# Kernel tuning notes

Hardware: AMD Instinct MI355X
Metric: run time of the kernel (lower is better)

The kernel has to match this reference:

```python
import jax, jax.numpy as jnp
import numpy as np

EPS = 1e-6

def rms_norm(x):
    return x * jax.lax.rsqrt(jnp.mean(x * x, axis=-1, keepdims=True) + EPS)

def setup_inputs() -> dict:
    key = jax.random.key(0)
    k_x, k_w = jax.random.split(key)
    T, B, D = 2048, 16, 1024
    x = jax.random.normal(k_x, (T, B, D), dtype=jnp.float32)
    h0 = jnp.zeros((B, D), dtype=jnp.float32)
    # xavier_uniform for W: limit = sqrt(6/(fan_in+fan_out)) = sqrt(6/(2D))
    limit = float(np.sqrt(6.0 / (2 * D)))
    W = jax.random.uniform(k_w, (D, D), dtype=jnp.float32, minval=-limit, maxval=limit)
    b = jnp.zeros((D,), dtype=jnp.float32)
    log_alpha = jnp.asarray(np.log(0.1), dtype=jnp.float32)
    return {"x": x, "h0": h0, "W": W, "b": b, "log_alpha": log_alpha}

def reference(x, h0, W, b, log_alpha):
    # x: [T,B,D], h0: [B,D], W: [D,D], b: [D], log_alpha: []
    alpha = jnp.exp(log_alpha)
    # Precompute all input projections in one big GEMM: [T,B,D]
    Wx_all = jnp.einsum('tbd,ed->tbe', x, W) + b

    def step(h, wx):
        h_new = rms_norm(h + alpha * wx)
        out = h_new * jax.nn.silu(h_new)
        return h_new, (h_new, out)

    _, (hs, outs) = jax.lax.scan(step, h0, Wx_all)
    h = jnp.concatenate([h0[None], hs], axis=0)  # [T+1,B,D]
    return outs, h
```

## Files before the change

kernel.cpp:

```cpp
#include <hip/hip_runtime.h>
#include <hip/hip_bf16.h>

#define T_STEPS 2048
#define BATCH 16
#define DIM 1024
#define EPSV 1e-6f
#define INVD (1.0f / 1024.0f)
#define SLOTF (BATCH * DIM)
#define SLOT4C (BATCH * DIM / 4)

typedef short short8 __attribute__((ext_vector_type(8)));
typedef float f32x4 __attribute__((ext_vector_type(4)));

struct alignas(16) bf16x8pack { __hip_bfloat16 v[8]; };

__device__ __forceinline__ float dot4(const float4& a, const float4& c) {
  return fmaf(a.x, c.x, fmaf(a.y, c.y, fmaf(a.z, c.z, a.w * c.w)));
}

__device__ __forceinline__ float fast_rsq(float x) {
  float r;
  asm("v_rsq_f32 %0, %1" : "=v"(r) : "v"(x));
  return r;
}

__global__ __launch_bounds__(256) void cvt_kernel(const float* __restrict__ src,
                                                  bf16x8pack* __restrict__ dst, int n8) {
  int i = blockIdx.x * blockDim.x + threadIdx.x;
  if (i >= n8) return;
  const float4* s4 = (const float4*)src + (size_t)i * 2;
  float4 a = s4[0];
  float4 b = s4[1];
  bf16x8pack p;
  p.v[0] = __float2bfloat16(a.x); p.v[1] = __float2bfloat16(a.y);
  p.v[2] = __float2bfloat16(a.z); p.v[3] = __float2bfloat16(a.w);
  p.v[4] = __float2bfloat16(b.x); p.v[5] = __float2bfloat16(b.y);
  p.v[6] = __float2bfloat16(b.z); p.v[7] = __float2bfloat16(b.w);
  dst[i] = p;
}

__global__ __launch_bounds__(256) void gemm_kernel(
    const __hip_bfloat16* __restrict__ Xb,
    const __hip_bfloat16* __restrict__ Wb,
    const float* __restrict__ bias,
    const float* __restrict__ log_alpha_p,
    float* __restrict__ hreg) {
  __shared__ __hip_bfloat16 As[128 * 32];
  __shared__ __hip_bfloat16 Bs[128 * 32];
  const int tid = threadIdx.x;
  const int wave = tid >> 6, lane = tid & 63;
  const int m0 = blockIdx.y * 128;
  const int e0 = blockIdx.x * 128;
  const int wm = (wave >> 1) * 64;
  const int wn = (wave & 1) * 64;
  const int l15 = lane & 15, l4 = lane >> 4;

  f32x4 acc[4][4] = {};

  const int srow = wave * 16 + (lane >> 2);
  const int sch = (lane & 3) * 8;

  for (int kt = 0; kt < DIM; kt += 32) {
    __syncthreads();
#pragma unroll
    for (int i = 0; i < 2; ++i) {
      const __hip_bfloat16* ga = Xb + (size_t)(m0 + i * 64 + srow) * DIM + kt + sch;
      const __hip_bfloat16* gb = Wb + (size_t)(e0 + i * 64 + srow) * DIM + kt + sch;
      __builtin_amdgcn_global_load_lds(
          (const __attribute__((address_space(1))) void*)ga,
          (__attribute__((address_space(3))) void*)((char*)As + (i * 64 + wave * 16) * 64),
          16, 0, 0);
      __builtin_amdgcn_global_load_lds(
          (const __attribute__((address_space(1))) void*)gb,
          (__attribute__((address_space(3))) void*)((char*)Bs + (i * 64 + wave * 16) * 64),
          16, 0, 0);
    }
    __syncthreads();
    short8 a[4], b[4];
#pragma unroll
    for (int f = 0; f < 4; ++f)
      a[f] = *(const short8*)((const char*)As + ((wm + f * 16 + l15) * 32 + l4 * 8) * 2);
#pragma unroll
    for (int g = 0; g < 4; ++g)
      b[g] = *(const short8*)((const char*)Bs + ((wn + g * 16 + l15) * 32 + l4 * 8) * 2);
#pragma unroll
    for (int f = 0; f < 4; ++f)
#pragma unroll
      for (int g = 0; g < 4; ++g)
        acc[f][g] = __builtin_amdgcn_mfma_f32_16x16x32_bf16(a[f], b[g], acc[f][g], 0, 0, 0);
  }
  const float alpha = __expf(log_alpha_p[0]);
#pragma unroll
  for (int g = 0; g < 4; ++g) {
    const int e = e0 + wn + g * 16 + l15;
    const float bv = bias[e];
#pragma unroll
    for (int f = 0; f < 4; ++f) {
#pragma unroll
      for (int r = 0; r < 4; ++r) {
        const int m = m0 + wm + f * 16 + l4 * 4 + r;
        hreg[(size_t)(m + BATCH) * DIM + e] = alpha * (acc[f][g][r] + bv);
      }
    }
  }
}

__device__ __forceinline__ float dpp_sum_reg(float x) {
  float acc = x;
#define DPP_ADD(ctrl)                                                              \
  {                                                                                \
    int t_ = __builtin_amdgcn_update_dpp(0, __float_as_int(acc), (ctrl), 0xf, 0xf, \
                                         true);                                    \
    acc += __int_as_float(t_);                                                     \
  }
  DPP_ADD(0x111); DPP_ADD(0x112); DPP_ADD(0x114); DPP_ADD(0x118);
  DPP_ADD(0x142); DPP_ADD(0x143);
#undef DPP_ADD
  return acc;
}

__global__ __launch_bounds__(64) void dots_kernel(const float* __restrict__ hreg,
                                                  float4* __restrict__ scal4,
                                                  float2* __restrict__ d45g) {
  const int t = blockIdx.x >> 4;
  const int b = blockIdx.x & 15;
  const int lane = threadIdx.x;
  const float4* w  = (const float4*)(hreg + (size_t)(t + 1) * SLOTF + b * DIM);
  const float4* m1 = (const float4*)(hreg + (size_t)(t    ) * SLOTF + b * DIM);
  const float4* m2 = (const float4*)(hreg + (size_t)(t - 1) * SLOTF + b * DIM);
  const float4* m3 = (const float4*)(hreg + (size_t)(t - 2) * SLOTF + b * DIM);
  const float4* m4 = (const float4*)(hreg + (size_t)(t - 3) * SLOTF + b * DIM);
  const float4* m5 = (const float4*)(hreg + (size_t)(t - 4) * SLOTF + b * DIM);
  float e = 0.f, d = 0.f, d2 = 0.f, d3 = 0.f, d4 = 0.f, d5 = 0.f;
#pragma unroll
  for (int j = 0; j < 4; ++j) {
    float4 a = w[lane + 64 * j];
    e = fmaf(a.x, a.x, fmaf(a.y, a.y, fmaf(a.z, a.z, fmaf(a.w, a.w, e))));
    if (t >= 1) { float4 p = m1[lane + 64 * j];
      d = fmaf(p.x, a.x, fmaf(p.y, a.y, fmaf(p.z, a.z, fmaf(p.w, a.w, d)))); }
    if (t >= 2) { float4 p = m2[lane + 64 * j];
      d2 = fmaf(p.x, a.x, fmaf(p.y, a.y, fmaf(p.z, a.z, fmaf(p.w, a.w, d2)))); }
    if (t >= 3) { float4 p = m3[lane + 64 * j];
      d3 = fmaf(p.x, a.x, fmaf(p.y, a.y, fmaf(p.z, a.z, fmaf(p.w, a.w, d3)))); }
    if (t >= 4) { float4 p = m4[lane + 64 * j];
      d4 = fmaf(p.x, a.x, fmaf(p.y, a.y, fmaf(p.z, a.z, fmaf(p.w, a.w, d4)))); }
    if (t >= 5) { float4 p = m5[lane + 64 * j];
      d5 = fmaf(p.x, a.x, fmaf(p.y, a.y, fmaf(p.z, a.z, fmaf(p.w, a.w, d5)))); }
  }
  e = dpp_sum_reg(e);
  d = dpp_sum_reg(d);
  d2 = dpp_sum_reg(d2);
  d3 = dpp_sum_reg(d3);
  d4 = dpp_sum_reg(d4);
  d5 = dpp_sum_reg(d5);
  if (lane == 63) {
    scal4[b * T_STEPS + t] = make_float4(e, d + d, d2 + d2, d3 + d3);
    d45g[b * T_STEPS + t] = make_float2(d4 + d4, d5 + d5);
  }
}

__global__ __launch_bounds__(256, 1) void scan_kernel(
    const float* __restrict__ h0,
    const float4* __restrict__ scal4,
    const float2* __restrict__ d45g,
    float* __restrict__ hreg) {
  const int b = blockIdx.x;
  const int tid = threadIdx.x;
  const int wave = tid >> 6;
  const int lane = tid & 63;
  float4* h4 = (float4*)hreg;
  const int idx4 = b * 256 + tid;

  __shared__ float4 scLDS[T_STEPS];
  __shared__ float2 d45LDS[T_STEPS];
  __shared__ alignas(16) float Gp[4][4];
  __shared__ float initP[4][6];

#pragma unroll
  for (int p = 0; p < 8; ++p)
    scLDS[p * 256 + tid] = scal4[b * T_STEPS + p * 256 + tid];
#pragma unroll
  for (int p = 0; p < 8; ++p)
    d45LDS[p * 256 + tid] = d45g[b * T_STEPS + p * 256 + tid];

  float4 w[16];
#pragma unroll
  for (int k = 2; k < 16; ++k) w[k] = h4[(size_t)SLOT4C * (k + 1) + idx4];
  w[0] = h4[(size_t)SLOT4C * 17 + idx4];
  w[1] = h4[(size_t)SLOT4C * 18 + idx4];
  float4 w0v = h4[(size_t)SLOT4C * 1 + idx4];
  float4 w1v = h4[(size_t)SLOT4C * 2 + idx4];
  float4 h0v = ((const float4*)h0)[idx4];
  h4[idx4] = h0v;

  float4 s;
  s.x = h0v.x + w0v.x; s.y = h0v.y + w0v.y;
  s.z = h0v.z + w0v.z; s.w = h0v.w + w0v.w;
  {
    float q  = dpp_sum_reg(dot4(s, s));
    float r  = dpp_sum_reg(dot4(s, w1v));
    float c2 = dpp_sum_reg(dot4(s, w[2]));
    float c3 = dpp_sum_reg(dot4(s, w[3]));
    float c4 = dpp_sum_reg(dot4(s, w[4]));
    float c5 = dpp_sum_reg(dot4(s, w[5]));
    if (lane == 63) {
      initP[wave][0] = q;  initP[wave][1] = r;  initP[wave][2] = c2;
      initP[wave][3] = c3; initP[wave][4] = c4; initP[wave][5] = c5;
    }
  }
  __syncthreads();
  const float n1 = (initP[0][0] + initP[1][0]) + (initP[2][0] + initP[3][0]);
  float t1 = (initP[0][1] + initP[1][1]) + (initP[2][1] + initP[3][1]);
  float t2 = (initP[0][2] + initP[1][2]) + (initP[2][2] + initP[3][2]);
  float t3 = (initP[0][3] + initP[1][3]) + (initP[2][3] + initP[3][3]);
  float t4 = (initP[0][4] + initP[1][4]) + (initP[2][4] + initP[3][4]);
  float t5 = (initP[0][5] + initP[1][5]) + (initP[2][5] + initP[3][5]);
  const float B1 = t1 + t1, C2 = t2 + t2, C3 = t3 + t3, C4 = t4 + t4, C5 = t5 + t5;

  const float e1 = scLDS[1].x;
  float4 sc2 = scLDS[2], sc3 = scLDS[3], sc4 = scLDS[4], sc5 = scLDS[5];
  const float D45x = d45LDS[5].x;
  float4 scA = scLDS[6], scB = scLDS[7];
  float2 d45A = d45LDS[6], d45B = d45LDS[7];

  float n = n1, rm1, rm2, rm3, rm4, pp;
  float gr0 = 0.f, gr1 = 0.f;
  float4 rv = make_float4(0.f, 0.f, 0.f, 0.f);
  float4 hvr[4];

#define BAR0 { asm volatile("s_waitcnt lgkmcnt(0)" ::: "memory"); __builtin_amdgcn_s_barrier(); }

  {
    const float rinv = fast_rsq(fmaf(n, INVD, EPSV));
    n = fmaf(rinv, fmaf(rinv, n, B1), e1);
    hvr[1].x = rinv * s.x; hvr[1].y = rinv * s.y;
    hvr[1].z = rinv * s.z; hvr[1].w = rinv * s.w;
    h4[(size_t)SLOT4C * 1 + idx4] = hvr[1];
    s.x = hvr[1].x + w1v.x; s.y = hvr[1].y + w1v.y;
    s.z = hvr[1].z + w1v.z; s.w = hvr[1].w + w1v.w;
    pp = dpp_sum_reg(dot4(hvr[1], w[6]));
    rm1 = rinv;
    BAR0
  }
  {
    if (lane == 63) Gp[2][wave] = pp;
    const float rinv = fast_rsq(fmaf(n, INVD, EPSV));
    const float BB = fmaf(rm1, C2, sc2.y);
    n = fmaf(rinv, fmaf(rinv, n, BB), sc2.x);
    hvr[2].x = rinv * s.x; hvr[2].y = rinv * s.y;
    hvr[2].z = rinv * s.z; hvr[2].w = rinv * s.w;
    h4[(size_t)SLOT4C * 2 + idx4] = hvr[2];
    s.x = hvr[2].x + w[2].x; s.y = hvr[2].y + w[2].y;
    s.z = hvr[2].z + w[2].z; s.w = hvr[2].w + w[2].w;
    pp = dpp_sum_reg(dot4(hvr[2], w[7]));
    w[2] = h4[(size_t)SLOT4C * 19 + idx4];
    rm2 = rm1; rm1 = rinv;
    BAR0
  }
  {
    if (lane == 63) Gp[3][wave] = pp;
    const float rinv = fast_rsq(fmaf(n, INVD, EPSV));
    const float BB = fmaf(rm1, fmaf(rm2, C3, sc3.z), sc3.y);
    n = fmaf(rinv, fmaf(rinv, n, BB), sc3.x);
    hvr[3].x = rinv * s.x; hvr[3].y = rinv * s.y;
    hvr[3].z = rinv * s.z; hvr[3].w = rinv * s.w;
    h4[(size_t)SLOT4C * 3 + idx4] = hvr[3];
    s.x = hvr[3].x + w[3].x; s.y = hvr[3].y + w[3].y;
    s.z = hvr[3].z + w[3].z; s.w = hvr[3].w + w[3].w;
    pp = dpp_sum_reg(dot4(hvr[3], w[8]));
    w[3] = h4[(size_t)SLOT4C * 20 + idx4];
    rm3 = rm2; rm2 = rm1; rm1 = rinv;
    BAR0
  }
  {
    if (lane == 63) Gp[0][wave] = pp;
    const float rinv = fast_rsq(fmaf(n, INVD, EPSV));
    const float BB = fmaf(rm1, fmaf(rm2, fmaf(rm3, C4, sc4.w), sc4.z), sc4.y);
    n = fmaf(rinv, fmaf(rinv, n, BB), sc4.x);
    rv = *(const float4*)&Gp[2][0];
    hvr[0].x = rinv * s.x; hvr[0].y = rinv * s.y;
    hvr[0].z = rinv * s.z; hvr[0].w = rinv * s.w;
    h4[(size_t)SLOT4C * 4 + idx4] = hvr[0];
    s.x = hvr[0].x + w[4].x; s.y = hvr[0].y + w[4].y;
    s.z = hvr[0].z + w[4].z; s.w = hvr[0].w + w[4].w;
    pp = dpp_sum_reg(dot4(hvr[0], w[9]));
    w[4] = h4[(size_t)SLOT4C * 21 + idx4];
    rm4 = rm3; rm3 = rm2; rm2 = rm1; rm1 = rinv;
    BAR0
  }
  {
    if (lane == 63) Gp[1][wave] = pp;
    const float rinv = fast_rsq(fmaf(n, INVD, EPSV));
    const float BB =
        fmaf(rm1, fmaf(rm2, fmaf(rm3, fmaf(rm4, C5, D45x), sc5.w), sc5.z), sc5.y);
    n = fmaf(rinv, fmaf(rinv, n, BB), sc5.x);
    { float gt = (rv.x + rv.y) + (rv.z + rv.w); gr0 = gt + gt; }
    rv = *(const float4*)&Gp[3][0];
    hvr[1].x = rinv * s.x; hvr[1].y = rinv * s.y;
    hvr[1].z = rinv * s.z; hvr[1].w = rinv * s.w;
    h4[(size_t)SLOT4C * 5 + idx4] = hvr[1];
    s.x = hvr[1].x + w[5].x; s.y = hvr[1].y + w[5].y;
    s.z = hvr[1].z + w[5].z; s.w = hvr[1].w + w[5].w;
    pp = dpp_sum_reg(dot4(hvr[1], w[10]));
    w[5] = h4[(size_t)SLOT4C * 22 + idx4];
    rm4 = rm3; rm3 = rm2; rm2 = rm1; rm1 = rinv;
    BAR0
  }

#define STEP(I_, WS, W5S, GW, GR, SCR, D45R, GRU, GRW, HVI, BAR_)                    \
  {                                                                                  \
    const int i_ = (I_);                                                             \
    if (lane == 63) Gp[GW][wave] = pp;                                               \
    { float gt_ = (rv.x + rv.y) + (rv.z + rv.w); GRW = gt_ + gt_; }                  \
    rv = *(const float4*)&Gp[GR][0];                                                 \
    const float rinv = fast_rsq(fmaf(n, INVD, EPSV));                                \
    const float BB = fmaf(                                                           \
        rm1, fmaf(rm2, fmaf(rm3, fmaf(rm4, (D45R).y + (GRU), (D45R).x), (SCR).w),    \
                  (SCR).z), (SCR).y);                                                \
    n = fmaf(rinv, fmaf(rinv, n, BB), (SCR).x);                                      \
    hvr[HVI].x = rinv * s.x; hvr[HVI].y = rinv * s.y;                                \
    hvr[HVI].z = rinv * s.z; hvr[HVI].w = rinv * s.w;                                \
    h4[(size_t)SLOT4C * i_ + idx4] = hvr[HVI];                                       \
    s.x = hvr[HVI].x + w[WS].x; s.y = hvr[HVI].y + w[WS].y;                          \
    s.z = hvr[HVI].z + w[WS].z; s.w = hvr[HVI].w + w[WS].w;                          \
    pp = dpp_sum_reg(dot4(hvr[HVI], w[W5S]));                                        \
    const int ipf_ = (i_ + 16 < T_STEPS) ? (i_ + 16) : (T_STEPS - 1);                \
    w[WS] = h4[(size_t)SLOT4C * (ipf_ + 1) + idx4];                                  \
    const int isc_ = (i_ + 2 < T_STEPS) ? (i_ + 2) : (T_STEPS - 1);                  \
    SCR = scLDS[isc_];                                                               \
    D45R = d45LDS[isc_];                                                             \
    rm4 = rm3; rm3 = rm2; rm2 = rm1; rm1 = rinv;                                     \
    if (BAR_) { asm volatile("s_waitcnt lgkmcnt(3)" ::: "memory");                   \
                __builtin_amdgcn_s_barrier(); }                                      \
  }

  for (int ii = 6; ii < 2038; ii += 16) {
    STEP(ii + 0,  6, 11, 2, 0, scA, d45A, gr0, gr1, 2, 0)
    STEP(ii + 1,  7, 12, 3, 1, scB, d45B, gr1, gr0, 3, 1)
    STEP(ii + 2,  8, 13, 0, 2, scA, d45A, gr0, gr1, 0, 0)
    STEP(ii + 3,  9, 14, 1, 3, scB, d45B, gr1, gr0, 1, 1)
    STEP(ii + 4, 10, 15, 2, 0, scA, d45A, gr0, gr1, 2, 0)
    STEP(ii + 5, 11,  0, 3, 1, scB, d45B, gr1, gr0, 3, 1)
    STEP(ii + 6, 12,  1, 0, 2, scA, d45A, gr0, gr1, 0, 0)
    STEP(ii + 7, 13,  2, 1, 3, scB, d45B, gr1, gr0, 1, 1)
    STEP(ii + 8, 14,  3, 2, 0, scA, d45A, gr0, gr1, 2, 0)
    STEP(ii + 9, 15,  4, 3, 1, scB, d45B, gr1, gr0, 3, 1)
    STEP(ii + 10, 0,  5, 0, 2, scA, d45A, gr0, gr1, 0, 0)
    STEP(ii + 11, 1,  6, 1, 3, scB, d45B, gr1, gr0, 1, 1)
    STEP(ii + 12, 2,  7, 2, 0, scA, d45A, gr0, gr1, 2, 0)
    STEP(ii + 13, 3,  8, 3, 1, scB, d45B, gr1, gr0, 3, 1)
    STEP(ii + 14, 4,  9, 0, 2, scA, d45A, gr0, gr1, 0, 0)
    STEP(ii + 15, 5, 10, 1, 3, scB, d45B, gr1, gr0, 1, 1)
  }
  STEP(2038,  6, 11, 2, 0, scA, d45A, gr0, gr1, 2, 0)
  STEP(2039,  7, 12, 3, 1, scB, d45B, gr1, gr0, 3, 1)
  STEP(2040,  8, 13, 0, 2, scA, d45A, gr0, gr1, 0, 0)
  STEP(2041,  9, 14, 1, 3, scB, d45B, gr1, gr0, 1, 1)
  STEP(2042, 10, 15, 2, 0, scA, d45A, gr0, gr1, 2, 0)
  STEP(2043, 11,  0, 3, 1, scB, d45B, gr1, gr0, 3, 1)
  STEP(2044, 12,  1, 0, 2, scA, d45A, gr0, gr1, 0, 0)
  STEP(2045, 13,  2, 1, 3, scB, d45B, gr1, gr0, 1, 1)
  STEP(2046, 14,  3, 2, 0, scA, d45A, gr0, gr1, 2, 0)
  STEP(2047, 15,  4, 3, 1, scB, d45B, gr1, gr0, 3, 1)
#undef STEP
#undef BAR0

  const float rinvT = fast_rsq(fmaf(n, INVD, EPSV));
  float4 o;
  o.x = rinvT * s.x; o.y = rinvT * s.y; o.z = rinvT * s.z; o.w = rinvT * s.w;
  h4[(size_t)SLOT4C * T_STEPS + idx4] = o;
}

__global__ __launch_bounds__(256) void silu_kernel(const float4* __restrict__ hsrc,
                                                   float4* __restrict__ out4, int n4) {
  int i = blockIdx.x * blockDim.x + threadIdx.x;
  if (i >= n4) return;
  float4 h = hsrc[i];
  float4 o;
  o.x = h.x * h.x / (1.f + __expf(-h.x));
  o.y = h.y * h.y / (1.f + __expf(-h.y));
  o.z = h.z * h.z / (1.f + __expf(-h.z));
  o.w = h.w * h.w / (1.f + __expf(-h.w));
  out4[i] = o;
}

extern "C" void kernel_launch(void* const* d_in, const int* in_sizes, int n_in,
                              void* d_out, int out_size, void* d_ws, size_t ws_size,
                              hipStream_t stream) {
  (void)in_sizes; (void)n_in; (void)d_ws; (void)ws_size; (void)out_size;
  const float* x = (const float*)d_in[0];
  const float* h0 = (const float*)d_in[1];
  const float* W = (const float*)d_in[2];
  const float* bias = (const float*)d_in[3];
  const float* log_alpha = (const float*)d_in[4];

  float* out = (float*)d_out;
  float* hreg = out + (size_t)T_STEPS * BATCH * DIM;
  __hip_bfloat16* xb = (__hip_bfloat16*)d_out;
  __hip_bfloat16* wb = (__hip_bfloat16*)((char*)d_out + (size_t)T_STEPS * BATCH * DIM * 2);
  float4* scal4 = (float4*)(out + (size_t)26 * 1024 * 1024);
  float2* d45g = (float2*)(out + (size_t)27 * 1024 * 1024);

  const int nx8 = T_STEPS * BATCH * DIM / 8;
  const int nw8 = DIM * DIM / 8;
  cvt_kernel<<<nx8 / 256, 256, 0, stream>>>(x, (bf16x8pack*)xb, nx8);
  cvt_kernel<<<nw8 / 256, 256, 0, stream>>>(W, (bf16x8pack*)wb, nw8);

  dim3 ggrid(DIM / 128, (T_STEPS * BATCH) / 128);
  gemm_kernel<<<ggrid, 256, 0, stream>>>(xb, wb, bias, log_alpha, hreg);

  dots_kernel<<<T_STEPS * BATCH, 64, 0, stream>>>(hreg, scal4, d45g);

  scan_kernel<<<BATCH, 256, 0, stream>>>(h0, scal4, d45g, hreg);

  const int n4 = T_STEPS * BATCH * DIM / 4;
  silu_kernel<<<n4 / 256, 256, 0, stream>>>((const float4*)(hreg + BATCH * DIM),
                                            (float4*)out, n4);
}
```

Measured before the change: 538.4 us.

## Stream Wx slabs via global_load_lds ring buffer instead of register prefetch

Replaces the 16-deep register-resident prefetch of Wx slices with a 12-slot LDS ring filled by asynchronous global_load_lds, and reads per-step scalar coefficients straight from global memory a few steps ahead instead of staging all of them into LDS up front. This frees many VGPRs and drops the upfront LDS staging pass. In exchange it adds LDS reads each step, vmcnt waits, and relies on correct counter bookkeeping across the serial scan.

```diff
diff --git a/kernel.cpp b/kernel.cpp
--- a/kernel.cpp
+++ b/kernel.cpp
@@ -17,7 +17,6 @@
 __device__ __forceinline__ float dot4(const float4& a, const float4& c) {
   return fmaf(a.x, c.x, fmaf(a.y, c.y, fmaf(a.z, c.z, a.w * c.w)));
 }
-
 __device__ __forceinline__ float fast_rsq(float x) {
   float r;
   asm("v_rsq_f32 %0, %1" : "=v"(r) : "v"(x));
@@ -171,38 +170,50 @@
   float4* h4 = (float4*)hreg;
   const int idx4 = b * 256 + tid;
 
-  __shared__ float4 scLDS[T_STEPS];
-  __shared__ float2 d45LDS[T_STEPS];
+  __shared__ float4 ldsW[12 * 256];
   __shared__ alignas(16) float Gp[4][4];
   __shared__ float initP[4][6];
 
-#pragma unroll
-  for (int p = 0; p < 8; ++p)
-    scLDS[p * 256 + tid] = scal4[b * T_STEPS + p * 256 + tid];
-#pragma unroll
-  for (int p = 0; p < 8; ++p)
-    d45LDS[p * 256 + tid] = d45g[b * T_STEPS + p * 256 + tid];
-
-  float4 w[16];
-#pragma unroll
-  for (int k = 2; k < 16; ++k) w[k] = h4[(size_t)SLOT4C * (k + 1) + idx4];
-  w[0] = h4[(size_t)SLOT4C * 17 + idx4];
-  w[1] = h4[(size_t)SLOT4C * 18 + idx4];
-  float4 w0v = h4[(size_t)SLOT4C * 1 + idx4];
-  float4 w1v = h4[(size_t)SLOT4C * 2 + idx4];
+#define GLD(SLOT, WIDX)                                                            \
+  __builtin_amdgcn_global_load_lds(                                                \
+      (const __attribute__((address_space(1))) void*)(hreg +                       \
+          (size_t)SLOTF * ((WIDX) + 1) + (size_t)idx4 * 4),                        \
+      (__attribute__((address_space(3))) void*)((char*)ldsW + (SLOT) * 4096 +      \
+                                                wave * 1024),                      \
+      16, 0, 0)
+
+  const float4* scg = scal4 + b * T_STEPS;
+  const float2* dg = d45g + b * T_STEPS;
+
+  GLD(0, 0); GLD(1, 1); GLD(2, 2); GLD(3, 3); GLD(4, 4); GLD(5, 5);
+  GLD(6, 6); GLD(7, 7); GLD(8, 8); GLD(9, 9); GLD(10, 10); GLD(11, 11);
   float4 h0v = ((const float4*)h0)[idx4];
+  const float e1 = scg[1].x;
+  float4 sc2v = scg[2], sc3v = scg[3], sc4v = scg[4], sc5v = scg[5];
+  const float D45x = dg[5].x;
+  float4 sc0_ = scg[8], sc1_ = scg[9], sc2_ = scg[6], sc3_ = scg[7];
+  float2 d0_ = dg[8], d1_ = dg[9], d2_ = dg[6], d3_ = dg[7];
+  asm volatile("s_waitcnt vmcnt(0)" ::: "memory");
+
+  float4 w0v = ldsW[0 * 256 + tid];
+  float4 w1v = ldsW[1 * 256 + tid];
+  float4 t2 = ldsW[2 * 256 + tid];
+  float4 t3 = ldsW[3 * 256 + tid];
+  float4 t4 = ldsW[4 * 256 + tid];
+  float4 t5 = ldsW[5 * 256 + tid];
+
   h4[idx4] = h0v;
-
   float4 s;
   s.x = h0v.x + w0v.x; s.y = h0v.y + w0v.y;
   s.z = h0v.z + w0v.z; s.w = h0v.w + w0v.w;
+
   {
     float q  = dpp_sum_reg(dot4(s, s));
     float r  = dpp_sum_reg(dot4(s, w1v));
-    float c2 = dpp_sum_reg(dot4(s, w[2]));
-    float c3 = dpp_sum_reg(dot4(s, w[3]));
-    float c4 = dpp_sum_reg(dot4(s, w[4]));
-    float c5 = dpp_sum_reg(dot4(s, w[5]));
+    float c2 = dpp_sum_reg(dot4(s, t2));
+    float c3 = dpp_sum_reg(dot4(s, t3));
+    float c4 = dpp_sum_reg(dot4(s, t4));
+    float c5 = dpp_sum_reg(dot4(s, t5));
     if (lane == 63) {
       initP[wave][0] = q;  initP[wave][1] = r;  initP[wave][2] = c2;
       initP[wave][3] = c3; initP[wave][4] = c4; initP[wave][5] = c5;
@@ -210,81 +221,74 @@
   }
   __syncthreads();
   const float n1 = (initP[0][0] + initP[1][0]) + (initP[2][0] + initP[3][0]);
-  float t1 = (initP[0][1] + initP[1][1]) + (initP[2][1] + initP[3][1]);
-  float t2 = (initP[0][2] + initP[1][2]) + (initP[2][2] + initP[3][2]);
-  float t3 = (initP[0][3] + initP[1][3]) + (initP[2][3] + initP[3][3]);
-  float t4 = (initP[0][4] + initP[1][4]) + (initP[2][4] + initP[3][4]);
-  float t5 = (initP[0][5] + initP[1][5]) + (initP[2][5] + initP[3][5]);
-  const float B1 = t1 + t1, C2 = t2 + t2, C3 = t3 + t3, C4 = t4 + t4, C5 = t5 + t5;
-
-  const float e1 = scLDS[1].x;
-  float4 sc2 = scLDS[2], sc3 = scLDS[3], sc4 = scLDS[4], sc5 = scLDS[5];
-  const float D45x = d45LDS[5].x;
-  float4 scA = scLDS[6], scB = scLDS[7];
-  float2 d45A = d45LDS[6], d45B = d45LDS[7];
+  float t1s = (initP[0][1] + initP[1][1]) + (initP[2][1] + initP[3][1]);
+  float t2s = (initP[0][2] + initP[1][2]) + (initP[2][2] + initP[3][2]);
+  float t3s = (initP[0][3] + initP[1][3]) + (initP[2][3] + initP[3][3]);
+  float t4s = (initP[0][4] + initP[1][4]) + (initP[2][4] + initP[3][4]);
+  float t5s = (initP[0][5] + initP[1][5]) + (initP[2][5] + initP[3][5]);
+  const float B1 = t1s + t1s, C2 = t2s + t2s, C3 = t3s + t3s,
+              C4 = t4s + t4s, C5 = t5s + t5s;
+  GLD(0, 12);
 
   float n = n1, rm1, rm2, rm3, rm4, pp;
   float gr0 = 0.f, gr1 = 0.f;
   float4 rv = make_float4(0.f, 0.f, 0.f, 0.f);
-  float4 hvr[4];
+  float4 hvE, hvO, wSa, wSb, wGa, wGb;
 
 #define BAR0 { asm volatile("s_waitcnt lgkmcnt(0)" ::: "memory"); __builtin_amdgcn_s_barrier(); }
 
   {
     const float rinv = fast_rsq(fmaf(n, INVD, EPSV));
     n = fmaf(rinv, fmaf(rinv, n, B1), e1);
-    hvr[1].x = rinv * s.x; hvr[1].y = rinv * s.y;
-    hvr[1].z = rinv * s.z; hvr[1].w = rinv * s.w;
-    h4[(size_t)SLOT4C * 1 + idx4] = hvr[1];
-    s.x = hvr[1].x + w1v.x; s.y = hvr[1].y + w1v.y;
-    s.z = hvr[1].z + w1v.z; s.w = hvr[1].w + w1v.w;
-    pp = dpp_sum_reg(dot4(hvr[1], w[6]));
+    hvO.x = rinv * s.x; hvO.y = rinv * s.y; hvO.z = rinv * s.z; hvO.w = rinv * s.w;
+    h4[(size_t)SLOT4C * 1 + idx4] = hvO;
+    s.x = hvO.x + w1v.x; s.y = hvO.y + w1v.y; s.z = hvO.z + w1v.z; s.w = hvO.w + w1v.w;
+    float4 wg = ldsW[6 * 256 + tid];
+    pp = dpp_sum_reg(dot4(hvO, wg));
+    GLD(1, 13);
     rm1 = rinv;
     BAR0
   }
   {
     if (lane == 63) Gp[2][wave] = pp;
     const float rinv = fast_rsq(fmaf(n, INVD, EPSV));
-    const float BB = fmaf(rm1, C2, sc2.y);
-    n = fmaf(rinv, fmaf(rinv, n, BB), sc2.x);
-    hvr[2].x = rinv * s.x; hvr[2].y = rinv * s.y;
-    hvr[2].z = rinv * s.z; hvr[2].w = rinv * s.w;
-    h4[(size_t)SLOT4C * 2 + idx4] = hvr[2];
-    s.x = hvr[2].x + w[2].x; s.y = hvr[2].y + w[2].y;
-    s.z = hvr[2].z + w[2].z; s.w = hvr[2].w + w[2].w;
-    pp = dpp_sum_reg(dot4(hvr[2], w[7]));
-    w[2] = h4[(size_t)SLOT4C * 19 + idx4];
+    const float BB = fmaf(rm1, C2, sc2v.y);
+    n = fmaf(rinv, fmaf(rinv, n, BB), sc2v.x);
+    hvE.x = rinv * s.x; hvE.y = rinv * s.y; hvE.z = rinv * s.z; hvE.w = rinv * s.w;
+    h4[(size_t)SLOT4C * 2 + idx4] = hvE;
+    s.x = hvE.x + t2.x; s.y = hvE.y + t2.y; s.z = hvE.z + t2.z; s.w = hvE.w + t2.w;
+    float4 wg = ldsW[7 * 256 + tid];
+    pp = dpp_sum_reg(dot4(hvE, wg));
+    GLD(2, 14);
     rm2 = rm1; rm1 = rinv;
     BAR0
   }
   {
     if (lane == 63) Gp[3][wave] = pp;
     const float rinv = fast_rsq(fmaf(n, INVD, EPSV));
-    const float BB = fmaf(rm1, fmaf(rm2, C3, sc3.z), sc3.y);
-    n = fmaf(rinv, fmaf(rinv, n, BB), sc3.x);
-    hvr[3].x = rinv * s.x; hvr[3].y = rinv * s.y;
-    hvr[3].z = rinv * s.z; hvr[3].w = rinv * s.w;
-    h4[(size_t)SLOT4C * 3 + idx4] = hvr[3];
-    s.x = hvr[3].x + w[3].x; s.y = hvr[3].y + w[3].y;
-    s.z = hvr[3].z + w[3].z; s.w = hvr[3].w + w[3].w;
-    pp = dpp_sum_reg(dot4(hvr[3], w[8]));
-    w[3] = h4[(size_t)SLOT4C * 20 + idx4];
+    const float BB = fmaf(rm1, fmaf(rm2, C3, sc3v.z), sc3v.y);
+    n = fmaf(rinv, fmaf(rinv, n, BB), sc3v.x);
+    hvO.x = rinv * s.x; hvO.y = rinv * s.y; hvO.z = rinv * s.z; hvO.w = rinv * s.w;
+    h4[(size_t)SLOT4C * 3 + idx4] = hvO;
+    s.x = hvO.x + t3.x; s.y = hvO.y + t3.y; s.z = hvO.z + t3.z; s.w = hvO.w + t3.w;
+    float4 wg = ldsW[8 * 256 + tid];
+    pp = dpp_sum_reg(dot4(hvO, wg));
+    GLD(3, 15);
     rm3 = rm2; rm2 = rm1; rm1 = rinv;
     BAR0
   }
   {
     if (lane == 63) Gp[0][wave] = pp;
     const float rinv = fast_rsq(fmaf(n, INVD, EPSV));
-    const float BB = fmaf(rm1, fmaf(rm2, fmaf(rm3, C4, sc4.w), sc4.z), sc4.y);
-    n = fmaf(rinv, fmaf(rinv, n, BB), sc4.x);
+    const float BB = fmaf(rm1, fmaf(rm2, fmaf(rm3, C4, sc4v.w), sc4v.z), sc4v.y);
+    n = fmaf(rinv, fmaf(rinv, n, BB), sc4v.x);
     rv = *(const float4*)&Gp[2][0];
-    hvr[0].x = rinv * s.x; hvr[0].y = rinv * s.y;
-    hvr[0].z = rinv * s.z; hvr[0].w = rinv * s.w;
-    h4[(size_t)SLOT4C * 4 + idx4] = hvr[0];
-    s.x = hvr[0].x + w[4].x; s.y = hvr[0].y + w[4].y;
-    s.z = hvr[0].z + w[4].z; s.w = hvr[0].w + w[4].w;
-    pp = dpp_sum_reg(dot4(hvr[0], w[9]));
-    w[4] = h4[(size_t)SLOT4C * 21 + idx4];
+    hvE.x = rinv * s.x; hvE.y = rinv * s.y; hvE.z = rinv * s.z; hvE.w = rinv * s.w;
+    h4[(size_t)SLOT4C * 4 + idx4] = hvE;
+    s.x = hvE.x + t4.x; s.y = hvE.y + t4.y; s.z = hvE.z + t4.z; s.w = hvE.w + t4.w;
+    float4 wg = ldsW[9 * 256 + tid];
+    pp = dpp_sum_reg(dot4(hvE, wg));
+    GLD(4, 16);
     rm4 = rm3; rm3 = rm2; rm2 = rm1; rm1 = rinv;
     BAR0
   }
@@ -292,78 +296,68 @@
     if (lane == 63) Gp[1][wave] = pp;
     const float rinv = fast_rsq(fmaf(n, INVD, EPSV));
     const float BB =
-        fmaf(rm1, fmaf(rm2, fmaf(rm3, fmaf(rm4, C5, D45x), sc5.w), sc5.z), sc5.y);
-    n = fmaf(rinv, fmaf(rinv, n, BB), sc5.x);
+        fmaf(rm1, fmaf(rm2, fmaf(rm3, fmaf(rm4, C5, D45x), sc5v.w), sc5v.z), sc5v.y);
+    n = fmaf(rinv, fmaf(rinv, n, BB), sc5v.x);
     { float gt = (rv.x + rv.y) + (rv.z + rv.w); gr0 = gt + gt; }
     rv = *(const float4*)&Gp[3][0];
-    hvr[1].x = rinv * s.x; hvr[1].y = rinv * s.y;
-    hvr[1].z = rinv * s.z; hvr[1].w = rinv * s.w;
-    h4[(size_t)SLOT4C * 5 + idx4] = hvr[1];
-    s.x = hvr[1].x + w[5].x; s.y = hvr[1].y + w[5].y;
-    s.z = hvr[1].z + w[5].z; s.w = hvr[1].w + w[5].w;
-    pp = dpp_sum_reg(dot4(hvr[1], w[10]));
-    w[5] = h4[(size_t)SLOT4C * 22 + idx4];
+    hvO.x = rinv * s.x; hvO.y = rinv * s.y; hvO.z = rinv * s.z; hvO.w = rinv * s.w;
+    h4[(size_t)SLOT4C * 5 + idx4] = hvO;
+    s.x = hvO.x + t5.x; s.y = hvO.y + t5.y; s.z = hvO.z + t5.z; s.w = hvO.w + t5.w;
+    float4 wg = ldsW[10 * 256 + tid];
+    pp = dpp_sum_reg(dot4(hvO, wg));
+    GLD(5, 17);
+    wSa = ldsW[6 * 256 + tid];
+    wGa = ldsW[11 * 256 + tid];
     rm4 = rm3; rm3 = rm2; rm2 = rm1; rm1 = rinv;
     BAR0
   }
-
-#define STEP(I_, WS, W5S, GW, GR, SCR, D45R, GRU, GRW, HVI, BAR_)                    \
+  asm volatile("s_waitcnt vmcnt(0)" ::: "memory");
+
+#define STEP(I_, SLW, SLG, SLP, GW, GR, SC, D45, GRU, GRW, WU, WGU, WP, WGP, HV, BAR_) \
   {                                                                                  \
     const int i_ = (I_);                                                             \
+    asm volatile("s_waitcnt vmcnt(22)" ::: "memory");                                \
     if (lane == 63) Gp[GW][wave] = pp;                                               \
     { float gt_ = (rv.x + rv.y) + (rv.z + rv.w); GRW = gt_ + gt_; }                  \
     rv = *(const float4*)&Gp[GR][0];                                                 \
+    WP = ldsW[(SLW) * 256 + tid];                                                    \
+    WGP = ldsW[(SLG) * 256 + tid];                                                   \
     const float rinv = fast_rsq(fmaf(n, INVD, EPSV));                                \
     const float BB = fmaf(                                                           \
-        rm1, fmaf(rm2, fmaf(rm3, fmaf(rm4, (D45R).y + (GRU), (D45R).x), (SCR).w),    \
-                  (SCR).z), (SCR).y);                                                \
-    n = fmaf(rinv, fmaf(rinv, n, BB), (SCR).x);                                      \
-    hvr[HVI].x = rinv * s.x; hvr[HVI].y = rinv * s.y;                                \
-    hvr[HVI].z = rinv * s.z; hvr[HVI].w = rinv * s.w;                                \
-    h4[(size_t)SLOT4C * i_ + idx4] = hvr[HVI];                                       \
-    s.x = hvr[HVI].x + w[WS].x; s.y = hvr[HVI].y + w[WS].y;                          \
-    s.z = hvr[HVI].z + w[WS].z; s.w = hvr[HVI].w + w[WS].w;                          \
-    pp = dpp_sum_reg(dot4(hvr[HVI], w[W5S]));                                        \
-    const int ipf_ = (i_ + 16 < T_STEPS) ? (i_ + 16) : (T_STEPS - 1);                \
-    w[WS] = h4[(size_t)SLOT4C * (ipf_ + 1) + idx4];                                  \
-    const int isc_ = (i_ + 2 < T_STEPS) ? (i_ + 2) : (T_STEPS - 1);                  \
-    SCR = scLDS[isc_];                                                               \
-    D45R = d45LDS[isc_];                                                             \
+        rm1, fmaf(rm2, fmaf(rm3, fmaf(rm4, (D45).y + (GRU), (D45).x), (SC).w),       \
+                  (SC).z), (SC).y);                                                  \
+    n = fmaf(rinv, fmaf(rinv, n, BB), (SC).x);                                       \
+    HV.x = rinv * s.x; HV.y = rinv * s.y; HV.z = rinv * s.z; HV.w = rinv * s.w;      \
+    h4[(size_t)SLOT4C * i_ + idx4] = HV;                                             \
+    s.x = HV.x + WU.x; s.y = HV.y + WU.y; s.z = HV.z + WU.z; s.w = HV.w + WU.w;      \
+    pp = dpp_sum_reg(dot4(HV, WGU));                                                 \
+    { const int wsrc_ = (i_ + 12 <= 2047) ? (i_ + 12) : 2047; GLD(SLP, wsrc_); }     \
+    { const int isc_ = (i_ + 4 <= 2047) ? (i_ + 4) : 2047;                           \
+      SC = scg[isc_]; D45 = dg[isc_]; }                                              \
     rm4 = rm3; rm3 = rm2; rm2 = rm1; rm1 = rinv;                                     \
     if (BAR_) { asm volatile("s_waitcnt lgkmcnt(3)" ::: "memory");                   \
                 __builtin_amdgcn_s_barrier(); }                                      \
   }
 
-  for (int ii = 6; ii < 2038; ii += 16) {
-    STEP(ii + 0,  6, 11, 2, 0, scA, d45A, gr0, gr1, 2, 0)
-    STEP(ii + 1,  7, 12, 3, 1, scB, d45B, gr1, gr0, 3, 1)
-    STEP(ii + 2,  8, 13, 0, 2, scA, d45A, gr0, gr1, 0, 0)
-    STEP(ii + 3,  9, 14, 1, 3, scB, d45B, gr1, gr0, 1, 1)
-    STEP(ii + 4, 10, 15, 2, 0, scA, d45A, gr0, gr1, 2, 0)
-    STEP(ii + 5, 11,  0, 3, 1, scB, d45B, gr1, gr0, 3, 1)
-    STEP(ii + 6, 12,  1, 0, 2, scA, d45A, gr0, gr1, 0, 0)
-    STEP(ii + 7, 13,  2, 1, 3, scB, d45B, gr1, gr0, 1, 1)
-    STEP(ii + 8, 14,  3, 2, 0, scA, d45A, gr0, gr1, 2, 0)
-    STEP(ii + 9, 15,  4, 3, 1, scB, d45B, gr1, gr0, 3, 1)
-    STEP(ii + 10, 0,  5, 0, 2, scA, d45A, gr0, gr1, 0, 0)
-    STEP(ii + 11, 1,  6, 1, 3, scB, d45B, gr1, gr0, 1, 1)
-    STEP(ii + 12, 2,  7, 2, 0, scA, d45A, gr0, gr1, 2, 0)
-    STEP(ii + 13, 3,  8, 3, 1, scB, d45B, gr1, gr0, 3, 1)
-    STEP(ii + 14, 4,  9, 0, 2, scA, d45A, gr0, gr1, 0, 0)
-    STEP(ii + 15, 5, 10, 1, 3, scB, d45B, gr1, gr0, 1, 1)
-  }
-  STEP(2038,  6, 11, 2, 0, scA, d45A, gr0, gr1, 2, 0)
-  STEP(2039,  7, 12, 3, 1, scB, d45B, gr1, gr0, 3, 1)
-  STEP(2040,  8, 13, 0, 2, scA, d45A, gr0, gr1, 0, 0)
-  STEP(2041,  9, 14, 1, 3, scB, d45B, gr1, gr0, 1, 1)
-  STEP(2042, 10, 15, 2, 0, scA, d45A, gr0, gr1, 2, 0)
-  STEP(2043, 11,  0, 3, 1, scB, d45B, gr1, gr0, 3, 1)
-  STEP(2044, 12,  1, 0, 2, scA, d45A, gr0, gr1, 0, 0)
-  STEP(2045, 13,  2, 1, 3, scB, d45B, gr1, gr0, 1, 1)
-  STEP(2046, 14,  3, 2, 0, scA, d45A, gr0, gr1, 2, 0)
-  STEP(2047, 15,  4, 3, 1, scB, d45B, gr1, gr0, 3, 1)
+  for (int ii = 6; ii <= 2034; ii += 12) {
+    STEP(ii + 0,  7,  0,  6, 2, 0, sc2_, d2_, gr0, gr1, wSa, wGa, wSb, wGb, hvE, 0)
+    STEP(ii + 1,  8,  1,  7, 3, 1, sc3_, d3_, gr1, gr0, wSb, wGb, wSa, wGa, hvO, 1)
+    STEP(ii + 2,  9,  2,  8, 0, 2, sc0_, d0_, gr0, gr1, wSa, wGa, wSb, wGb, hvE, 0)
+    STEP(ii + 3, 10,  3,  9, 1, 3, sc1_, d1_, gr1, gr0, wSb, wGb, wSa, wGa, hvO, 1)
+    STEP(ii + 4, 11,  4, 10, 2, 0, sc2_, d2_, gr0, gr1, wSa, wGa, wSb, wGb, hvE, 0)
+    STEP(ii + 5,  0,  5, 11, 3, 1, sc3_, d3_, gr1, gr0, wSb, wGb, wSa, wGa, hvO, 1)
+    STEP(ii + 6,  1,  6,  0, 0, 2, sc0_, d0_, gr0, gr1, wSa, wGa, wSb, wGb, hvE, 0)
+    STEP(ii + 7,  2,  7,  1, 1, 3, sc1_, d1_, gr1, gr0, wSb, wGb, wSa, wGa, hvO, 1)
+    STEP(ii + 8,  3,  8,  2, 2, 0, sc2_, d2_, gr0, gr1, wSa, wGa, wSb, wGb, hvE, 0)
+    STEP(ii + 9,  4,  9,  3, 3, 1, sc3_, d3_, gr1, gr0, wSb, wGb, wSa, wGa, hvO, 1)
+    STEP(ii + 10, 5, 10,  4, 0, 2, sc0_, d0_, gr0, gr1, wSa, wGa, wSb, wGb, hvE, 0)
+    STEP(ii + 11, 6, 11,  5, 1, 3, sc1_, d1_, gr1, gr0, wSb, wGb, wSa, wGa, hvO, 1)
+  }
+  STEP(2046, 7, 0, 6, 2, 0, sc2_, d2_, gr0, gr1, wSa, wGa, wSb, wGb, hvE, 0)
+  STEP(2047, 8, 1, 7, 3, 1, sc3_, d3_, gr1, gr0, wSb, wGb, wSa, wGa, hvO, 1)
 #undef STEP
 #undef BAR0
+#undef GLD
 
   const float rinvT = fast_rsq(fmaf(n, INVD, EPSV));
   float4 o;
```

After: 706.3 us. 1.31x slower.
